# Optimization experiments

Measured on AMD Instinct MI355X. Metric: run time of the kernel, lower is better.

## Reference

```python
import jax, jax.numpy as jnp
import numpy as np

THRESHOLD = 1.0
DECAY = 0.95
T, B, N_IN = 16, 512, 3072
S1, S2, S3 = 256, 256, 128
E = 8


def _lif_step(v, h):
    # LIF membrane update: decay, integrate, threshold-spike, soft reset.
    v = v * DECAY + h
    spk = (v >= THRESHOLD).astype(v.dtype)
    return spk, v - spk * THRESHOLD


def setup_inputs() -> dict:
    key = jax.random.key(0)
    k_seq, k1, k2, k3 = jax.random.split(key, 4)
    # Binary spike train input (rate-coded), shape (T, B, N_in)
    spike_seq = (jax.random.uniform(k_seq, (T, B, N_IN)) < 0.5).astype(jnp.float32)
    # Expert weights: nn.Linear weight layout is (out, in); init N(0, 0.05)
    W1 = 0.05 * jax.random.normal(k1, (E, S1, N_IN), dtype=jnp.float32)
    W2 = 0.05 * jax.random.normal(k2, (E, S2, S1), dtype=jnp.float32)
    W3 = 0.05 * jax.random.normal(k3, (E, S3, S2), dtype=jnp.float32)
    # Uniform gates 1/num_experts (requires_grad=False buffers in the original)
    g = jnp.full((E,), 1.0 / E, dtype=jnp.float32)
    return {"spike_seq": spike_seq, "W1": W1, "W2": W2, "W3": W3,
            "g1": g, "g2": g, "g3": g}


def reference(spike_seq, W1, W2, W3, g1, g2, g3):
    t, b = spike_seq.shape[0], spike_seq.shape[1]
    x = spike_seq.reshape(t, b, -1)
    e = W1.shape[0]
    dt = x.dtype
    v1 = jnp.zeros((e, b, W1.shape[1]), dt)
    v2 = jnp.zeros((e, b, W2.shape[1]), dt)
    v3 = jnp.zeros((e, b, W3.shape[1]), dt)

    def step(carry, xt):
        v1, v2, v3 = carry
        # stage 1: batched per-expert GEMM + LIF + gated combine
        h1 = jnp.einsum('bi,eoi->ebo', xt, W1)
        spk1, v1 = _lif_step(v1, h1)
        c1 = jnp.einsum('e,ebo->bo', g1, spk1)
        # stage 2
        h2 = jnp.einsum('bi,eoi->ebo', c1, W2)
        spk2, v2 = _lif_step(v2, h2)
        c2 = jnp.einsum('e,ebo->bo', g2, spk2)
        # stage 3
        h3 = jnp.einsum('bi,eoi->ebo', c2, W3)
        spk3, v3 = _lif_step(v3, h3)
        c3 = jnp.einsum('e,ebo->bo', g3, spk3)
        return (v1, v2, v3), (c1, c2, c3)

    _, (s1, s2, s3) = jax.lax.scan(step, (v1, v2, v3), x)
    # time-averaged combined outputs per stage
    return s1.mean(axis=0), s2.mean(axis=0), s3.mean(axis=0)
```

## Files before the change

### kernel.cpp

```cpp
#include <hip/hip_runtime.h>
#include <hip/hip_bf16.h>
#include <cmath>

#define T_STEPS 16
#define BATCH   512
#define N_IN    3072
#define S1      256
#define S2      256
#define S3      128
#define NEXP    8
#define M_ROWS  (T_STEPS * BATCH)
#define MT_ALL  (M_ROWS / 32)

typedef int v4i  __attribute__((ext_vector_type(4)));
typedef int v16i __attribute__((ext_vector_type(16)));
typedef unsigned long long u64;
typedef unsigned int uint32;

__device__ __forceinline__ v4i unpack16_bits(uint32 w16)
{
    v4i d;
    #pragma unroll
    for (int c = 0; c < 4; ++c)
        d[c] = (int)((((w16 >> (4 * c)) & 0xFu) * 0x00204081u) & 0x01010101u);
    return d;
}

template<int S, int K>
__device__ __forceinline__ void digitize_chunk(
    const float* __restrict__ W, char* __restrict__ Bf, int t)
{
    int lane16 = t & 63;
    int o  = (t >> 6) & (S - 1);
    int kb = t >> ((S == 256) ? 14 : 13);
    int r  = lane16 & 31;
    int qd = lane16 >> 5;
    int e    = r >> 2;
    int limb = r & 3;
    int k0 = kb * 32 + qd * 16;

    const float4* Wp = (const float4*)(W + ((size_t)e * S + o) * K + k0);
    char out[16];
    #pragma unroll
    for (int f4 = 0; f4 < 4; ++f4) {
        float4 w = Wp[f4];
        float ws[4] = {w.x, w.y, w.z, w.w};
        #pragma unroll
        for (int c = 0; c < 4; ++c) {
            long long q = llrint((double)ws[c] * 4294967296.0);
            int d = 0;
            #pragma unroll
            for (int l = 0; l < 4; ++l) {
                int dl = (int)((q + 128) & 255) - 128;
                q = (q - dl) >> 8;
                if (l == limb) d = dl;
            }
            out[f4 * 4 + c] = (char)d;
        }
    }
    *(v4i*)(Bf + (size_t)t * 16) = *(v4i*)out;
}

__global__ __launch_bounds__(256) void prep(
    const float* __restrict__ x,  const float* __restrict__ W1,
    const float* __restrict__ W2, const float* __restrict__ W3,
    u64* __restrict__ bitsT, char* __restrict__ B1f,
    char* __restrict__ B2f,  char* __restrict__ B3f)
{
    const int bid = blockIdx.x;
    const int tid = threadIdx.x;
    if (bid < 98304) {
        int gid = bid * 256 + tid;
        float v = x[gid];
        u64 m = __ballot(v >= 0.5f);
        if ((tid & 63) == 0) {
            int tb = gid / N_IN;
            int k  = gid - tb * N_IN;
            int t  = tb >> 9;
            int b  = tb & 511;
            bitsT[(size_t)(k >> 6) * M_ROWS + (b * 16 + t)] = m;
        }
    } else if (bid < 98304 + 6144) {
        digitize_chunk<S1, N_IN>(W1, B1f, (bid - 98304) * 256 + tid);
    } else if (bid < 98304 + 6144 + 512) {
        digitize_chunk<S2, S1>(W2, B2f, (bid - 98304 - 6144) * 256 + tid);
    } else {
        digitize_chunk<S3, S2>(W3, B3f, (bid - 98304 - 6656) * 256 + tid);
    }
}

template<int K, int S, int SHIFT, bool ABITS, bool WRITEC, int NBLK, int MINW>
__global__ __launch_bounds__(256, MINW) void fused_stage(
    const void* __restrict__ Ap, const char* __restrict__ Bf,
    const float* __restrict__ g, char* __restrict__ Cf,
    float* __restrict__ Mean)
{
    constexpr int KI = K / 64;
    static_assert(KI % 2 == 0, "KI must be even");
    constexpr int NT = S;
    constexpr int NS = NBLK / 8;
    __shared__ double hs[256][16];

    const int tid  = threadIdx.x;
    const int lane = tid & 63;
    const int w    = tid >> 6;
    const int col  = lane & 31;
    const int qd   = lane >> 5;
    const int wm   = w * 64;

    const int id   = blockIdx.x;
    const int nblk = (id & 7) * NS + ((id >> 3) % NS);
    const int mblk = id / NBLK;
    const int m0   = mblk * 256;

    const int nt0 = nblk * 2;
    const char* Bbase = Bf + ((size_t)nt0 * 64 + lane) * 16;

    v16i acc[2][2];
    #pragma unroll
    for (int i = 0; i < 2; ++i)
        #pragma unroll
        for (int j = 0; j < 2; ++j)
            #pragma unroll
            for (int r = 0; r < 16; ++r) acc[i][j][r] = 0;

    auto loadB = [&](int kb, int jj) -> v4i {
        return *(const v4i*)(Bbase + (size_t)kb * (NT * 1024) + jj * 1024);
    };

    v4i Bb[2][4];

    if constexpr (ABITS) {
        const u64* AT = (const u64*)Ap + (m0 + wm + col);
        const int sh16 = qd * 16;
        u64 a0b[2], a1b[2];

        a0b[0] = AT[0];
        a1b[0] = AT[32];
        #pragma unroll
        for (int ks = 0; ks < 2; ++ks)
            #pragma unroll
            for (int jj = 0; jj < 2; ++jj)
                Bb[0][ks * 2 + jj] = loadB(ks, jj);

        auto body = [&](int it, int cur, int pf) {
            const int itp = it + 1;
            a0b[pf] = AT[(size_t)itp * M_ROWS];
            a1b[pf] = AT[(size_t)itp * M_ROWS + 32];
            #pragma unroll
            for (int ks = 0; ks < 2; ++ks)
                #pragma unroll
                for (int jj = 0; jj < 2; ++jj)
                    Bb[pf][ks * 2 + jj] = loadB(itp * 2 + ks, jj);
            __builtin_amdgcn_s_setprio(1);
            #pragma unroll
            for (int ks = 0; ks < 2; ++ks) {
                uint32 dw0 = ks ? (uint32)(a0b[cur] >> 32) : (uint32)a0b[cur];
                uint32 dw1 = ks ? (uint32)(a1b[cur] >> 32) : (uint32)a1b[cur];
                v4i af0 = unpack16_bits(dw0 >> sh16);
                v4i af1 = unpack16_bits(dw1 >> sh16);
                #pragma unroll
                for (int jj = 0; jj < 2; ++jj) {
                    acc[0][jj] = __builtin_amdgcn_mfma_i32_32x32x32_i8(af0, Bb[cur][ks*2+jj], acc[0][jj], 0,0,0);
                    acc[1][jj] = __builtin_amdgcn_mfma_i32_32x32x32_i8(af1, Bb[cur][ks*2+jj], acc[1][jj], 0,0,0);
                }
            }
            __builtin_amdgcn_s_setprio(0);
        };
        for (int it = 0; it < KI; it += 2) {
            body(it + 0, 0, 1);
            body(it + 1, 1, 0);
        }
    } else {
        const int mt0 = (m0 + wm) >> 5;
        const char* Abase = (const char*)Ap + ((size_t)mt0 * 64 + lane) * 16;
        auto loadA = [&](int kb, int ii) -> v4i {
            return *(const v4i*)(Abase + (size_t)kb * (MT_ALL * 1024) + ii * 1024);
        };
        v4i Ab[2][4];

        #pragma unroll
        for (int ks = 0; ks < 2; ++ks) {
            Ab[0][ks * 2 + 0] = loadA(ks, 0);
            Ab[0][ks * 2 + 1] = loadA(ks, 1);
            #pragma unroll
            for (int jj = 0; jj < 2; ++jj)
                Bb[0][ks * 2 + jj] = loadB(ks, jj);
        }

        auto body = [&](int it, int cur, int pf) {
            const int itp = it + 1;
            #pragma unroll
            for (int ks = 0; ks < 2; ++ks) {
                Ab[pf][ks * 2 + 0] = loadA(itp * 2 + ks, 0);
                Ab[pf][ks * 2 + 1] = loadA(itp * 2 + ks, 1);
                #pragma unroll
                for (int jj = 0; jj < 2; ++jj)
                    Bb[pf][ks * 2 + jj] = loadB(itp * 2 + ks, jj);
            }
            __builtin_amdgcn_s_setprio(1);
            #pragma unroll
            for (int ks = 0; ks < 2; ++ks)
                #pragma unroll
                for (int jj = 0; jj < 2; ++jj) {
                    acc[0][jj] = __builtin_amdgcn_mfma_i32_32x32x32_i8(Ab[cur][ks*2+0], Bb[cur][ks*2+jj], acc[0][jj], 0,0,0);
                    acc[1][jj] = __builtin_amdgcn_mfma_i32_32x32x32_i8(Ab[cur][ks*2+1], Bb[cur][ks*2+jj], acc[1][jj], 0,0,0);
                }
            __builtin_amdgcn_s_setprio(0);
        };
        for (int it = 0; it < KI; it += 2) {
            body(it + 0, 0, 1);
            body(it + 1, 1, 0);
        }
    }

    const double sbase = 1.0 / (double)(1ll << SHIFT);
    #pragma unroll
    for (int j = 0; j < 2; ++j) {
        const int oe = j * 8 + (col >> 2);
        #pragma unroll
        for (int i = 0; i < 2; ++i) {
            #pragma unroll
            for (int reg = 0; reg < 16; ++reg) {
                int a = acc[i][j][reg];
                int s01 = a + (__shfl_xor(a, 1) << 8);
                int s23 = __shfl_xor(s01, 2);
                double d = ((double)s01 + 65536.0 * (double)s23) * sbase;
                if ((col & 3) == 0) {
                    int m = wm + i * 32 + (reg & 3) + 8 * (reg >> 2) + 4 * qd;
                    hs[m][oe] = d;
                }
            }
        }
    }
    __syncthreads();

    const int b_loc  = tid >> 4;
    const int o_loc  = (tid >> 3) & 1;
    const int e      = tid & 7;
    const int oe     = o_loc * 8 + e;
    const float ge   = g[e];
    const int bg = mblk * 16 + b_loc;
    const int og = nblk * 2 + o_loc;

    const int kb_a   = og >> 5;
    const int qd_a   = (og >> 4) & 1;
    const int byte_a = og & 15;

    double v = 0.0;
    float gacc = 0.0f;
    #pragma unroll
    for (int t = 0; t < T_STEPS; ++t) {
        double h  = hs[b_loc * 16 + t][oe];
        double vv = v * 0.95 + h;
        int spk = (vv >= 1.0) ? 1 : 0;
        v = vv - (double)spk;
        float gs = ge * (float)spk;
        gs += __shfl_xor(gs, 1);
        gs += __shfl_xor(gs, 2);
        gs += __shfl_xor(gs, 4);
        gacc += gs;
        if (WRITEC) {
            int cnt = spk;
            cnt += __shfl_xor(cnt, 1);
            cnt += __shfl_xor(cnt, 2);
            cnt += __shfl_xor(cnt, 4);
            if (e == 0) {
                int mp = bg * 16 + t;
                int lane_a = (mp & 31) + 32 * qd_a;
                Cf[(((size_t)kb_a * MT_ALL + (mp >> 5)) * 64 + lane_a) * 16 + byte_a]
                    = (char)cnt;
            }
        }
    }
    if (e == 0) Mean[(size_t)bg * S + og] = gacc * 0.0625f;
}

extern "C" void kernel_launch(void* const* d_in, const int* in_sizes, int n_in,
                              void* d_out, int out_size, void* d_ws, size_t ws_size,
                              hipStream_t stream) {
    const float* x  = (const float*)d_in[0];
    const float* W1 = (const float*)d_in[1];
    const float* W2 = (const float*)d_in[2];
    const float* W3 = (const float*)d_in[3];
    const float* g1 = (const float*)d_in[4];
    const float* g2 = (const float*)d_in[5];
    const float* g3 = (const float*)d_in[6];
    float* out = (float*)d_out;

    char* ws = (char*)d_ws;
    u64*  AbitsT = (u64*)ws;
    char* B1f    = ws + 4194304ull;
    char* B2f    = ws + 31457280ull;
    char* B3f    = ws + 34603008ull;
    char* c1f    = ws + 36175872ull;
    char* c2f    = ws + 39321600ull;

    dim3 blk(256);

    prep<<<98304 + 6144 + 512 + 256, blk, 0, stream>>>(
        x, W1, W2, W3, AbitsT, B1f, B2f, B3f);

    fused_stage<N_IN, S1, 32, true,  true,  128, 4><<<32 * 128, blk, 0, stream>>>(
        AbitsT, B1f, g1, c1f, out);
    fused_stage<S1,   S2, 35, false, true,  128, 3><<<32 * 128, blk, 0, stream>>>(
        c1f, B2f, g2, c2f, out + BATCH * S1);
    fused_stage<S2,   S3, 35, false, false, 64, 3><<<32 * 64, blk, 0, stream>>>(
        c2f, B3f, g3, nullptr, out + BATCH * (S1 + S2));
}
```

Before: 518.5 us.

## Parameterize per-wave GEMM tile shape and use 32x128 wave tiles in stage one

Templates the fused stage kernel on per-wave M and N tile sizes, replacing the fixed 64x64 wave tile. Stage one switches to 32x128 wave tiles with 128-row blocks and a 64x64 grid, so each unpacked bit-plane A fragment feeds four MFMAs instead of two. The cost is twice as many weight-fragment loads per MFMA. The change also drops the s_setprio hints around the MFMA loops and rewrites the bit-unpack multiply as shift-adds.

```diff
diff --git a/kernel.cpp b/kernel.cpp
--- a/kernel.cpp
+++ b/kernel.cpp
@@ -21,8 +21,12 @@
 {
     v4i d;
     #pragma unroll
-    for (int c = 0; c < 4; ++c)
-        d[c] = (int)((((w16 >> (4 * c)) & 0xFu) * 0x00204081u) & 0x01010101u);
+    for (int c = 0; c < 4; ++c) {
+        uint32 x = (w16 >> (4 * c)) & 0xFu;
+        x = x + (x << 7);
+        x = x + (x << 14);
+        d[c] = (int)(x & 0x01010101u);
+    }
     return d;
 }
 
@@ -89,38 +93,42 @@
     }
 }
 
-template<int K, int S, int SHIFT, bool ABITS, bool WRITEC, int NBLK, int MINW>
+template<int K, int S, int SHIFT, bool ABITS, bool WRITEC,
+         int WM, int WN, int NBLK, int MINW>
 __global__ __launch_bounds__(256, MINW) void fused_stage(
     const void* __restrict__ Ap, const char* __restrict__ Bf,
     const float* __restrict__ g, char* __restrict__ Cf,
     float* __restrict__ Mean)
 {
-    constexpr int KI = K / 64;
+    constexpr int KI  = K / 64;
     static_assert(KI % 2 == 0, "KI must be even");
-    constexpr int NT = S;
-    constexpr int NS = NBLK / 8;
-    __shared__ double hs[256][16];
+    constexpr int MTW = WM / 32;
+    constexpr int NTW = WN / 32;
+    constexpr int BM  = 4 * WM;
+    constexpr int NT  = S;
+    constexpr int NS  = NBLK / 8;
+    __shared__ double hs[BM][8 * NTW];
 
     const int tid  = threadIdx.x;
     const int lane = tid & 63;
     const int w    = tid >> 6;
     const int col  = lane & 31;
     const int qd   = lane >> 5;
-    const int wm   = w * 64;
+    const int wm   = w * WM;
 
     const int id   = blockIdx.x;
     const int nblk = (id & 7) * NS + ((id >> 3) % NS);
     const int mblk = id / NBLK;
-    const int m0   = mblk * 256;
-
-    const int nt0 = nblk * 2;
+    const int m0   = mblk * BM;
+
+    const int nt0 = nblk * NTW;
     const char* Bbase = Bf + ((size_t)nt0 * 64 + lane) * 16;
 
-    v16i acc[2][2];
-    #pragma unroll
-    for (int i = 0; i < 2; ++i)
-        #pragma unroll
-        for (int j = 0; j < 2; ++j)
+    v16i acc[MTW][NTW];
+    #pragma unroll
+    for (int i = 0; i < MTW; ++i)
+        #pragma unroll
+        for (int j = 0; j < NTW; ++j)
             #pragma unroll
             for (int r = 0; r < 16; ++r) acc[i][j][r] = 0;
 
@@ -128,44 +136,47 @@
         return *(const v4i*)(Bbase + (size_t)kb * (NT * 1024) + jj * 1024);
     };
 
-    v4i Bb[2][4];
+    v4i Bb[2][2 * NTW];
 
     if constexpr (ABITS) {
         const u64* AT = (const u64*)Ap + (m0 + wm + col);
         const int sh16 = qd * 16;
-        u64 a0b[2], a1b[2];
-
-        a0b[0] = AT[0];
-        a1b[0] = AT[32];
+        u64 ab[2][MTW];
+
+        #pragma unroll
+        for (int mt = 0; mt < MTW; ++mt) ab[0][mt] = AT[mt * 32];
         #pragma unroll
         for (int ks = 0; ks < 2; ++ks)
             #pragma unroll
-            for (int jj = 0; jj < 2; ++jj)
-                Bb[0][ks * 2 + jj] = loadB(ks, jj);
+            for (int jj = 0; jj < NTW; ++jj)
+                Bb[0][ks * NTW + jj] = loadB(ks, jj);
 
         auto body = [&](int it, int cur, int pf) {
             const int itp = it + 1;
-            a0b[pf] = AT[(size_t)itp * M_ROWS];
-            a1b[pf] = AT[(size_t)itp * M_ROWS + 32];
+            #pragma unroll
+            for (int mt = 0; mt < MTW; ++mt)
+                ab[pf][mt] = AT[(size_t)itp * M_ROWS + mt * 32];
             #pragma unroll
             for (int ks = 0; ks < 2; ++ks)
                 #pragma unroll
-                for (int jj = 0; jj < 2; ++jj)
-                    Bb[pf][ks * 2 + jj] = loadB(itp * 2 + ks, jj);
-            __builtin_amdgcn_s_setprio(1);
+                for (int jj = 0; jj < NTW; ++jj)
+                    Bb[pf][ks * NTW + jj] = loadB(itp * 2 + ks, jj);
             #pragma unroll
             for (int ks = 0; ks < 2; ++ks) {
-                uint32 dw0 = ks ? (uint32)(a0b[cur] >> 32) : (uint32)a0b[cur];
-                uint32 dw1 = ks ? (uint32)(a1b[cur] >> 32) : (uint32)a1b[cur];
-                v4i af0 = unpack16_bits(dw0 >> sh16);
-                v4i af1 = unpack16_bits(dw1 >> sh16);
-                #pragma unroll
-                for (int jj = 0; jj < 2; ++jj) {
-                    acc[0][jj] = __builtin_amdgcn_mfma_i32_32x32x32_i8(af0, Bb[cur][ks*2+jj], acc[0][jj], 0,0,0);
-                    acc[1][jj] = __builtin_amdgcn_mfma_i32_32x32x32_i8(af1, Bb[cur][ks*2+jj], acc[1][jj], 0,0,0);
+                v4i af[MTW];
+                #pragma unroll
+                for (int mt = 0; mt < MTW; ++mt) {
+                    uint32 dw = ks ? (uint32)(ab[cur][mt] >> 32)
+                                   : (uint32)ab[cur][mt];
+                    af[mt] = unpack16_bits(dw >> sh16);
                 }
-            }
-            __builtin_amdgcn_s_setprio(0);
+                #pragma unroll
+                for (int mt = 0; mt < MTW; ++mt)
+                    #pragma unroll
+                    for (int jj = 0; jj < NTW; ++jj)
+                        acc[mt][jj] = __builtin_amdgcn_mfma_i32_32x32x32_i8(
+                            af[mt], Bb[cur][ks * NTW + jj], acc[mt][jj], 0,0,0);
+            }
         };
         for (int it = 0; it < KI; it += 2) {
             body(it + 0, 0, 1);
@@ -177,36 +188,38 @@
         auto loadA = [&](int kb, int ii) -> v4i {
             return *(const v4i*)(Abase + (size_t)kb * (MT_ALL * 1024) + ii * 1024);
         };
-        v4i Ab[2][4];
+        v4i Ab[2][2 * MTW];
 
         #pragma unroll
         for (int ks = 0; ks < 2; ++ks) {
-            Ab[0][ks * 2 + 0] = loadA(ks, 0);
-            Ab[0][ks * 2 + 1] = loadA(ks, 1);
-            #pragma unroll
-            for (int jj = 0; jj < 2; ++jj)
-                Bb[0][ks * 2 + jj] = loadB(ks, jj);
+            #pragma unroll
+            for (int mt = 0; mt < MTW; ++mt)
+                Ab[0][ks * MTW + mt] = loadA(ks, mt);
+            #pragma unroll
+            for (int jj = 0; jj < NTW; ++jj)
+                Bb[0][ks * NTW + jj] = loadB(ks, jj);
         }
 
         auto body = [&](int it, int cur, int pf) {
             const int itp = it + 1;
             #pragma unroll
             for (int ks = 0; ks < 2; ++ks) {
-                Ab[pf][ks * 2 + 0] = loadA(itp * 2 + ks, 0);
-                Ab[pf][ks * 2 + 1] = loadA(itp * 2 + ks, 1);
-                #pragma unroll
-                for (int jj = 0; jj < 2; ++jj)
-                    Bb[pf][ks * 2 + jj] = loadB(itp * 2 + ks, jj);
-            }
-            __builtin_amdgcn_s_setprio(1);
+                #pragma unroll
+                for (int mt = 0; mt < MTW; ++mt)
+                    Ab[pf][ks * MTW + mt] = loadA(itp * 2 + ks, mt);
+                #pragma unroll
+                for (int jj = 0; jj < NTW; ++jj)
+                    Bb[pf][ks * NTW + jj] = loadB(itp * 2 + ks, jj);
+            }
             #pragma unroll
             for (int ks = 0; ks < 2; ++ks)
                 #pragma unroll
-                for (int jj = 0; jj < 2; ++jj) {
-                    acc[0][jj] = __builtin_amdgcn_mfma_i32_32x32x32_i8(Ab[cur][ks*2+0], Bb[cur][ks*2+jj], acc[0][jj], 0,0,0);
-                    acc[1][jj] = __builtin_amdgcn_mfma_i32_32x32x32_i8(Ab[cur][ks*2+1], Bb[cur][ks*2+jj], acc[1][jj], 0,0,0);
-                }
-            __builtin_amdgcn_s_setprio(0);
+                for (int mt = 0; mt < MTW; ++mt)
+                    #pragma unroll
+                    for (int jj = 0; jj < NTW; ++jj)
+                        acc[mt][jj] = __builtin_amdgcn_mfma_i32_32x32x32_i8(
+                            Ab[cur][ks * MTW + mt], Bb[cur][ks * NTW + jj],
+                            acc[mt][jj], 0,0,0);
         };
         for (int it = 0; it < KI; it += 2) {
             body(it + 0, 0, 1);
@@ -216,10 +229,10 @@
 
     const double sbase = 1.0 / (double)(1ll << SHIFT);
     #pragma unroll
-    for (int j = 0; j < 2; ++j) {
+    for (int j = 0; j < NTW; ++j) {
         const int oe = j * 8 + (col >> 2);
         #pragma unroll
-        for (int i = 0; i < 2; ++i) {
+        for (int i = 0; i < MTW; ++i) {
             #pragma unroll
             for (int reg = 0; reg < 16; ++reg) {
                 int a = acc[i][j][reg];
@@ -235,13 +248,13 @@
     }
     __syncthreads();
 
-    const int b_loc  = tid >> 4;
-    const int o_loc  = (tid >> 3) & 1;
+    const int b_loc  = tid >> (3 + (NTW == 2 ? 1 : 2));
+    const int o_loc  = (tid >> 3) & (NTW - 1);
     const int e      = tid & 7;
     const int oe     = o_loc * 8 + e;
     const float ge   = g[e];
-    const int bg = mblk * 16 + b_loc;
-    const int og = nblk * 2 + o_loc;
+    const int bg = mblk * (BM / 16) + b_loc;
+    const int og = nblk * NTW + o_loc;
 
     const int kb_a   = og >> 5;
     const int qd_a   = (og >> 4) & 1;
@@ -301,10 +314,10 @@
     prep<<<98304 + 6144 + 512 + 256, blk, 0, stream>>>(
         x, W1, W2, W3, AbitsT, B1f, B2f, B3f);
 
-    fused_stage<N_IN, S1, 32, true,  true,  128, 4><<<32 * 128, blk, 0, stream>>>(
-        AbitsT, B1f, g1, c1f, out);
-    fused_stage<S1,   S2, 35, false, true,  128, 3><<<32 * 128, blk, 0, stream>>>(
-        c1f, B2f, g2, c2f, out + BATCH * S1);
-    fused_stage<S2,   S3, 35, false, false, 64, 3><<<32 * 64, blk, 0, stream>>>(
-        c2f, B3f, g3, nullptr, out + BATCH * (S1 + S2));
-}
+    fused_stage<N_IN, S1, 32, true,  true,  32, 128, 64, 3>
+        <<<64 * 64, blk, 0, stream>>>(AbitsT, B1f, g1, c1f, out);
+    fused_stage<S1,   S2, 35, false, true,  64, 64, 128, 3>
+        <<<32 * 128, blk, 0, stream>>>(c1f, B2f, g2, c2f, out + BATCH * S1);
+    fused_stage<S2,   S3, 35, false, false, 64, 64, 64, 3>
+        <<<32 * 64, blk, 0, stream>>>(c2f, B3f, g3, nullptr, out + BATCH * (S1 + S2));
+}
```

New measurement: 621.9 us. 1.2x slower.
